# Kernel tuning notes

Hardware: AMD Instinct MI355X
Metric: run time of the kernel (lower is better)

Reference implementation:

```python
import jax, jax.numpy as jnp
import numpy as np

D_MODEL = 1024
NUM_HEADS = 16
HEAD_DIM = D_MODEL // NUM_HEADS


def setup_inputs() -> dict:
    key = jax.random.key(0)
    ks = jax.random.split(key, 10)
    B, SQ, SKV = 4, 2048, 2048
    s = 1.0 / np.sqrt(D_MODEL)
    return {
        "query": jax.random.normal(ks[0], (B, SQ, D_MODEL), jnp.float32),
        "key_value": jax.random.normal(ks[1], (B, SKV, D_MODEL), jnp.float32),
        "Wq": jax.random.normal(ks[2], (D_MODEL, D_MODEL), jnp.float32) * s,
        "bq": jnp.zeros((D_MODEL,), jnp.float32),
        "Wk": jax.random.normal(ks[3], (D_MODEL, D_MODEL), jnp.float32) * s,
        "bk": jnp.zeros((D_MODEL,), jnp.float32),
        "Wv": jax.random.normal(ks[4], (D_MODEL, D_MODEL), jnp.float32) * s,
        "bv": jnp.zeros((D_MODEL,), jnp.float32),
        "Wo": jax.random.normal(ks[5], (D_MODEL, D_MODEL), jnp.float32) * s,
        "bo": jnp.zeros((D_MODEL,), jnp.float32),
    }


def reference(query, key_value, Wq, bq, Wk, bk, Wv, bv, Wo, bo):
    B, SQ, _ = query.shape
    SKV = key_value.shape[1]
    H, Dh = NUM_HEADS, HEAD_DIM
    # projections (torch Linear: x @ W.T + b); split heads -> (B, H, S, Dh)
    Q = (query @ Wq.T + bq).reshape(B, SQ, H, Dh).transpose(0, 2, 1, 3)
    K = (key_value @ Wk.T + bk).reshape(B, SKV, H, Dh).transpose(0, 2, 1, 3)
    V = (key_value @ Wv.T + bv).reshape(B, SKV, H, Dh).transpose(0, 2, 1, 3)
    scale = jnp.asarray(np.sqrt(Dh), query.dtype)
    scores = jnp.einsum("bhqd,bhkd->bhqk", Q, K) / scale
    weights = jax.nn.softmax(scores, axis=-1)  # dropout is identity in eval
    attn = jnp.einsum("bhqk,bhkd->bhqd", weights, V)
    attn = attn.transpose(0, 2, 1, 3).reshape(B, SQ, H * Dh)
    return attn @ Wo.T + bo
```

## Files before the change

kernel.cpp:

```cpp
#include <hip/hip_runtime.h>

#define NH 16
#define DH 64
#define DM 1024
#define SEQ 2048
#define BATCH 4

typedef short s16x8 __attribute__((ext_vector_type(8)));
typedef float f32x4 __attribute__((ext_vector_type(4)));

__device__ __forceinline__ unsigned short f2bf(float f) {
  union { float f; unsigned int u; } v; v.f = f;
  unsigned int u = v.u;
  unsigned int r = (u + 0x7fffu + ((u >> 16) & 1u)) >> 16;
  return (unsigned short)r;
}

__device__ __forceinline__ unsigned int pkbf(float a, float b) {
#if __has_builtin(__builtin_amdgcn_cvt_pk_bf16_f32)
  typedef short v2s __attribute__((ext_vector_type(2)));
  v2s r = __builtin_amdgcn_cvt_pk_bf16_f32(a, b);
  union { v2s v; unsigned int u; } cv; cv.v = r;
  return cv.u;
#else
  return (unsigned int)f2bf(a) | ((unsigned int)f2bf(b) << 16);
#endif
}

__device__ __forceinline__ float fexp2(float x) {
#if __has_builtin(__builtin_amdgcn_exp2f)
  return __builtin_amdgcn_exp2f(x);
#else
  return exp2f(x);
#endif
}

__device__ __forceinline__ void gload_lds16(const void* g, void* l) {
  __builtin_amdgcn_global_load_lds(
      (const __attribute__((address_space(1))) unsigned int*)g,
      (__attribute__((address_space(3))) unsigned int*)l, 16, 0, 0);
}

__global__ void convert_all(const float* __restrict__ q, const float* __restrict__ kv,
                            const float* __restrict__ w0, const float* __restrict__ w1,
                            const float* __restrict__ w2, const float* __restrict__ w3,
                            unsigned short* __restrict__ oq, unsigned short* __restrict__ okv,
                            unsigned short* __restrict__ ow0, unsigned short* __restrict__ ow1,
                            unsigned short* __restrict__ ow2, unsigned short* __restrict__ ow3) {
  const int NQ4 = (BATCH * SEQ * DM) / 4;
  const int NW4 = (DM * DM) / 4;
  const int total = NQ4 * 2 + NW4 * 4;
  for (int i = blockIdx.x * blockDim.x + threadIdx.x; i < total;
       i += gridDim.x * blockDim.x) {
    const float* s; unsigned short* d; int off;
    if (i < NQ4)            { s = q;  d = oq;  off = i; }
    else if (i < 2 * NQ4)   { s = kv; d = okv; off = i - NQ4; }
    else {
      int j = i - 2 * NQ4; int wsel = j / NW4; off = j - wsel * NW4;
      s = (wsel == 0) ? w0 : (wsel == 1) ? w1 : (wsel == 2) ? w2 : w3;
      d = (wsel == 0) ? ow0 : (wsel == 1) ? ow1 : (wsel == 2) ? ow2 : ow3;
    }
    float4 v = *(const float4*)(s + (size_t)off * 4);
    ushort4 o;
    o.x = f2bf(v.x); o.y = f2bf(v.y); o.z = f2bf(v.z); o.w = f2bf(v.w);
    *(ushort4*)(d + (size_t)off * 4) = o;
  }
}

__device__ __forceinline__ void gemm_tile(const unsigned short* __restrict__ X,
                                          const unsigned short* __restrict__ Wt,
                                          unsigned short* As, unsigned short* Bs,
                                          int m0, int n0, f32x4 (*acc)[4]) {
  const int tid = threadIdx.x;
  const int wv_ = tid >> 6, lane = tid & 63;
  const int quad = lane >> 4, c = lane & 15;
  const int wm = (wv_ >> 1) * 64, wn = (wv_ & 1) * 64;
  const int srow = lane >> 3;
  const int scol = ((lane & 7) ^ srow) * 8;

  for (int kt = 0; kt < DM; kt += 64) {
#pragma unroll
    for (int i = 0; i < 4; ++i) {
      int reg = wv_ * 4 + i;
      gload_lds16(X + (size_t)(m0 + reg * 8 + srow) * DM + kt + scol,
                  (void*)(As + reg * 512));
      gload_lds16(Wt + (size_t)(n0 + reg * 8 + srow) * DM + kt + scol,
                  (void*)(Bs + reg * 512));
    }
    __syncthreads();
#pragma unroll
    for (int k2 = 0; k2 < 2; ++k2) {
      s16x8 a[4], b[4];
      int g = k2 * 4 + quad;
#pragma unroll
      for (int t = 0; t < 4; ++t)
        a[t] = *(const s16x8*)(As + (wm + t * 16 + c) * 64 + ((g ^ (c & 7)) * 8));
#pragma unroll
      for (int t = 0; t < 4; ++t)
        b[t] = *(const s16x8*)(Bs + (wn + t * 16 + c) * 64 + ((g ^ (c & 7)) * 8));
#pragma unroll
      for (int tm = 0; tm < 4; ++tm)
#pragma unroll
        for (int tn = 0; tn < 4; ++tn)
          acc[tm][tn] = __builtin_amdgcn_mfma_f32_16x16x32_bf16(
              a[tm], b[tn], acc[tm][tn], 0, 0, 0);
    }
    __syncthreads();
  }
}

__global__ __launch_bounds__(256)
void gemm_qkv(const unsigned short* __restrict__ Xq,
              const unsigned short* __restrict__ Xkv,
              const unsigned short* __restrict__ W0,
              const unsigned short* __restrict__ W1,
              const unsigned short* __restrict__ W2,
              const float* __restrict__ b0, const float* __restrict__ b1,
              const float* __restrict__ b2,
              unsigned short* __restrict__ OQ, unsigned short* __restrict__ OK_,
              unsigned short* __restrict__ OV) {
  __shared__ alignas(16) unsigned short As[128 * 64];
  __shared__ alignas(16) unsigned short Bs[128 * 64];
  const int wg = blockIdx.x;
  const int L = (wg & 7) * 192 + (wg >> 3);
  const int m0 = (L & 63) * 128;
  const int yy = L >> 6;
  const int ysel = yy >> 3;
  const int n0 = (yy & 7) * 128;
  const unsigned short* X = (ysel == 0) ? Xq : Xkv;
  const unsigned short* Wt = (ysel == 0) ? W0 : (ysel == 1) ? W1 : W2;
  const float* bias = (ysel == 0) ? b0 : (ysel == 1) ? b1 : b2;
  unsigned short* Out = (ysel == 0) ? OQ : (ysel == 1) ? OK_ : OV;
  const float scale = (ysel == 0) ? 0.1803368801f : 1.0f;

  f32x4 acc[4][4] = {};
  gemm_tile(X, Wt, As, Bs, m0, n0, acc);

  const int tid = threadIdx.x;
  const int wv_ = tid >> 6, lane = tid & 63;
  const int quad = lane >> 4, c = lane & 15;
  const int wm = (wv_ >> 1) * 64, wn = (wv_ & 1) * 64;
#pragma unroll
  for (int tm = 0; tm < 4; ++tm) {
#pragma unroll
    for (int tn = 0; tn < 4; ++tn) {
      int n = n0 + wn + tn * 16 + c;
      float bv = bias[n];
      int m_base = m0 + wm + tm * 16 + quad * 4;
      if (ysel == 2) {
        int b_ = m_base >> 11, s_ = m_base & 2047, h_ = n >> 6, dh = n & 63;
        size_t idx = (((size_t)(b_ * NH + h_)) * DH + dh) * SEQ + s_;
        ushort4 o4;
        o4.x = f2bf(acc[tm][tn][0] + bv);
        o4.y = f2bf(acc[tm][tn][1] + bv);
        o4.z = f2bf(acc[tm][tn][2] + bv);
        o4.w = f2bf(acc[tm][tn][3] + bv);
        *(ushort4*)(&Out[idx]) = o4;
      } else {
#pragma unroll
        for (int p = 0; p < 4; ++p) {
          int m = m_base + p;
          float val = (acc[tm][tn][p] + bv) * scale;
          int b_ = m >> 11, s_ = m & 2047, h_ = n >> 6, dh = n & 63;
          size_t idx = (((size_t)(b_ * NH + h_)) * SEQ + s_) * DH + dh;
          Out[idx] = f2bf(val);
        }
      }
    }
  }
}

__global__ __launch_bounds__(256)
void gemm_o(const unsigned short* __restrict__ X,
            const unsigned short* __restrict__ Wt,
            const float* __restrict__ bias, float* __restrict__ Out) {
  __shared__ alignas(16) unsigned short As[128 * 64];
  __shared__ alignas(16) unsigned short Bs[128 * 64];
  const int wg = blockIdx.x;
  const int L = (wg & 7) * 64 + (wg >> 3);
  const int m0 = (L & 63) * 128;
  const int n0 = (L >> 6) * 128;
  f32x4 acc[4][4] = {};
  gemm_tile(X, Wt, As, Bs, m0, n0, acc);

  const int tid = threadIdx.x;
  const int wv_ = tid >> 6, lane = tid & 63;
  const int quad = lane >> 4, c = lane & 15;
  const int wm = (wv_ >> 1) * 64, wn = (wv_ & 1) * 64;
#pragma unroll
  for (int tm = 0; tm < 4; ++tm) {
#pragma unroll
    for (int tn = 0; tn < 4; ++tn) {
      int n = n0 + wn + tn * 16 + c;
      float bv = bias[n];
#pragma unroll
      for (int p = 0; p < 4; ++p) {
        int m = m0 + wm + tm * 16 + quad * 4 + p;
        Out[(size_t)m * DM + n] = acc[tm][tn][p] + bv;
      }
    }
  }
}

__global__ __launch_bounds__(512, 2)
void attn_kernel(const unsigned short* __restrict__ Qb,
                 const unsigned short* __restrict__ Kb,
                 const unsigned short* __restrict__ VTb,
                 unsigned short* __restrict__ Ob) {
  __shared__ alignas(16) unsigned short SM[18432];

  const int tid = threadIdx.x, wv_ = tid >> 6, lane = tid & 63;
  const int quad = lane >> 4, c = lane & 15;
  const int wg = blockIdx.x;
  const int bh = (wg & 7) + 8 * ((wg >> 3) >> 2);
  const int qb = (wg >> 3) & 3;
  const unsigned short* Qp = Qb + (size_t)bh * SEQ * DH;
  const unsigned short* Kp = Kb + (size_t)bh * SEQ * DH;
  const unsigned short* Vp = VTb + (size_t)bh * DH * SEQ;
  const int wq0 = qb * 512 + wv_ * 64;

  s16x8 aq[4][2];
#pragma unroll
  for (int t = 0; t < 4; ++t)
#pragma unroll
    for (int k2 = 0; k2 < 2; ++k2)
      aq[t][k2] = *(const s16x8*)(Qp + (size_t)(wq0 + t * 16 + c) * DH +
                                  k2 * 32 + quad * 8);

  f32x4 ot[4][4] = {};
  f32x4 lacc[4] = {};
  s16x8 ones;
  {
    union { s16x8 v; unsigned short u[8]; } o_;
#pragma unroll
    for (int j = 0; j < 8; ++j) o_.u[j] = 0x3F80;
    ones = o_.v;
  }

  const int srow = lane >> 3;
  const int schunk = (lane & 7) ^ srow;

#pragma unroll
  for (int i = 0; i < 2; ++i) {
    int slab = wv_ * 2 + i;
    if (slab < 8) {
      gload_lds16(Kp + (size_t)(slab * 8 + srow) * DH + schunk * 8,
                  (void*)(SM + slab * 512));
    } else {
      int s2 = slab - 8;
      gload_lds16(Vp + (size_t)(s2 * 8 + srow) * SEQ + schunk * 8,
                  (void*)(SM + 8192 + s2 * 512));
    }
  }

  for (int kt = 0; kt < SEQ; kt += 64) {
    const int cur = (kt >> 6) & 1;
    __syncthreads();
    if (kt + 64 < SEQ) {
      const int nxt = cur ^ 1;
#pragma unroll
      for (int i = 0; i < 2; ++i) {
        int slab = wv_ * 2 + i;
        if (slab < 8) {
          gload_lds16(Kp + (size_t)(kt + 64 + slab * 8 + srow) * DH + schunk * 8,
                      (void*)(SM + nxt * 4096 + slab * 512));
        } else {
          int s2 = slab - 8;
          gload_lds16(Vp + (size_t)(s2 * 8 + srow) * SEQ + kt + 64 + schunk * 8,
                      (void*)(SM + 8192 + nxt * 4096 + s2 * 512));
        }
      }
    }
    const unsigned short* K_ = SM + cur * 4096;
    const unsigned short* V_ = SM + 8192 + cur * 4096;

    f32x4 s[4][2][2] = {};
#pragma unroll
    for (int k2 = 0; k2 < 2; ++k2) {
      s16x8 ak[2][2];
#pragma unroll
      for (int jp = 0; jp < 2; ++jp)
#pragma unroll
        for (int h = 0; h < 2; ++h) {
          int r = jp * 32 + ((c >> 2) << 3) + h * 4 + (c & 3);
          int g = k2 * 4 + quad;
          ak[jp][h] = *(const s16x8*)(K_ + r * 64 + ((g ^ (r & 7)) * 8));
        }
#pragma unroll
      for (int t = 0; t < 4; ++t)
#pragma unroll
        for (int jp = 0; jp < 2; ++jp)
#pragma unroll
          for (int h = 0; h < 2; ++h)
            s[t][jp][h] = __builtin_amdgcn_mfma_f32_16x16x32_bf16(
                ak[jp][h], aq[t][k2], s[t][jp][h], 0, 0, 0);
    }

    s16x8 bp[4][2];
#pragma unroll
    for (int t = 0; t < 4; ++t)
#pragma unroll
      for (int jp = 0; jp < 2; ++jp) {
        float e00 = fexp2(s[t][jp][0][0]);
        float e01 = fexp2(s[t][jp][0][1]);
        float e02 = fexp2(s[t][jp][0][2]);
        float e03 = fexp2(s[t][jp][0][3]);
        float e10 = fexp2(s[t][jp][1][0]);
        float e11 = fexp2(s[t][jp][1][1]);
        float e12 = fexp2(s[t][jp][1][2]);
        float e13 = fexp2(s[t][jp][1][3]);
        union { s16x8 v; unsigned int u[4]; } pk;
        pk.u[0] = pkbf(e00, e01);
        pk.u[1] = pkbf(e02, e03);
        pk.u[2] = pkbf(e10, e11);
        pk.u[3] = pkbf(e12, e13);
        bp[t][jp] = pk.v;
        lacc[t] = __builtin_amdgcn_mfma_f32_16x16x32_bf16(
            ones, bp[t][jp], lacc[t], 0, 0, 0);
      }

#pragma unroll
    for (int jp = 0; jp < 2; ++jp)
#pragma unroll
      for (int dt = 0; dt < 4; ++dt) {
        int g = jp * 4 + quad;
        int r = dt * 16 + c;
        s16x8 av = *(const s16x8*)(V_ + r * 64 + ((g ^ (r & 7)) * 8));
#pragma unroll
        for (int t = 0; t < 4; ++t)
          ot[dt][t] = __builtin_amdgcn_mfma_f32_16x16x32_bf16(
              av, bp[t][jp], ot[dt][t], 0, 0, 0);
      }
  }

  __syncthreads();

  const int b_ = bh >> 4, h_ = bh & 15;
  const int ql = lane >> 1, hf = lane & 1;
  unsigned short* Lq = SM + wv_ * (32 * 72);
#pragma unroll
  for (int half = 0; half < 2; ++half) {
    if (half) asm volatile("s_waitcnt lgkmcnt(0)" ::: "memory");
#pragma unroll
    for (int t2 = 0; t2 < 2; ++t2) {
      int t = half * 2 + t2;
      float inv = 1.0f / lacc[t][0];
#pragma unroll
      for (int dt = 0; dt < 4; ++dt) {
        unsigned int w01 = pkbf(ot[dt][t][0] * inv, ot[dt][t][1] * inv);
        unsigned int w23 = pkbf(ot[dt][t][2] * inv, ot[dt][t][3] * inv);
        unsigned short* p = Lq + (t2 * 16 + c) * 72 + dt * 16 + quad * 4;
        *(unsigned int*)(p) = w01;
        *(unsigned int*)(p + 2) = w23;
      }
    }
    const unsigned short* Lr = Lq + ql * 72 + hf * 32;
    unsigned short* Og = Ob + ((size_t)(b_ * SEQ + wq0 + half * 32 + ql)) * DM +
                         h_ * 64 + hf * 32;
#pragma unroll
    for (int j = 0; j < 4; ++j) {
      s16x8 v = *(const s16x8*)(Lr + j * 8);
      *(s16x8*)(Og + j * 8) = v;
    }
  }
}

extern "C" void kernel_launch(void* const* d_in, const int* in_sizes, int n_in,
                              void* d_out, int out_size, void* d_ws, size_t ws_size,
                              hipStream_t stream) {
  const float* q  = (const float*)d_in[0];
  const float* kv = (const float*)d_in[1];
  const float* Wq = (const float*)d_in[2];
  const float* bq = (const float*)d_in[3];
  const float* Wk = (const float*)d_in[4];
  const float* bk = (const float*)d_in[5];
  const float* Wv = (const float*)d_in[6];
  const float* bv = (const float*)d_in[7];
  const float* Wo = (const float*)d_in[8];
  const float* bo = (const float*)d_in[9];

  char* ws = (char*)d_ws;
  const size_t MB = 1024 * 1024;
  unsigned short* q_bf  = (unsigned short*)(ws);
  unsigned short* kv_bf = (unsigned short*)(ws + 16 * MB);
  unsigned short* wq_bf = (unsigned short*)(ws + 32 * MB);
  unsigned short* wk_bf = (unsigned short*)(ws + 34 * MB);
  unsigned short* wv_bf = (unsigned short*)(ws + 36 * MB);
  unsigned short* wo_bf = (unsigned short*)(ws + 38 * MB);
  unsigned short* Qb    = (unsigned short*)(ws + 40 * MB);
  unsigned short* Kb    = (unsigned short*)(ws + 56 * MB);
  unsigned short* VTb   = (unsigned short*)(ws + 72 * MB);
  unsigned short* attn  = (unsigned short*)(ws + 88 * MB);

  convert_all<<<2048, 256, 0, stream>>>(q, kv, Wq, Wk, Wv, Wo,
                                        q_bf, kv_bf, wq_bf, wk_bf, wv_bf, wo_bf);
  gemm_qkv<<<dim3(1536), 256, 0, stream>>>(q_bf, kv_bf, wq_bf, wk_bf, wv_bf,
                                           bq, bk, bv, Qb, Kb, VTb);
  attn_kernel<<<dim3(256), 512, 0, stream>>>(Qb, Kb, VTb, attn);
  gemm_o<<<dim3(512), 256, 0, stream>>>(attn, wo_bf, bo, (float*)d_out);
}
```

Before: 325.7 us.

## Change LDS swizzle for K/V tiles and drop XCD-aware block remapping in GEMMs

Replaces the LDS XOR swizzle for the K and V tiles in attention. The old one XORed the 16-byte chunk index with the row index mod 8; the new one uses a pattern matched to the MFMA read lane mapping (fK, fV) and applies the same pattern on the global-to-LDS store side. The aim is fewer LDS bank conflicts on the fragment reads. Separately, the QKV and output GEMMs go back to a plain 2D grid without the XCD-interleaved block index remap. That may hurt L2 locality across the chiplets.

```diff
diff --git a/kernel.cpp b/kernel.cpp
--- a/kernel.cpp
+++ b/kernel.cpp
@@ -121,12 +121,9 @@
               unsigned short* __restrict__ OV) {
   __shared__ alignas(16) unsigned short As[128 * 64];
   __shared__ alignas(16) unsigned short Bs[128 * 64];
-  const int wg = blockIdx.x;
-  const int L = (wg & 7) * 192 + (wg >> 3);
-  const int m0 = (L & 63) * 128;
-  const int yy = L >> 6;
-  const int ysel = yy >> 3;
-  const int n0 = (yy & 7) * 128;
+  const int m0 = blockIdx.x * 128;
+  const int ysel = blockIdx.y >> 3;
+  const int n0 = (blockIdx.y & 7) * 128;
   const unsigned short* X = (ysel == 0) ? Xq : Xkv;
   const unsigned short* Wt = (ysel == 0) ? W0 : (ysel == 1) ? W1 : W2;
   const float* bias = (ysel == 0) ? b0 : (ysel == 1) ? b1 : b2;
@@ -176,10 +173,8 @@
             const float* __restrict__ bias, float* __restrict__ Out) {
   __shared__ alignas(16) unsigned short As[128 * 64];
   __shared__ alignas(16) unsigned short Bs[128 * 64];
-  const int wg = blockIdx.x;
-  const int L = (wg & 7) * 64 + (wg >> 3);
-  const int m0 = (L & 63) * 128;
-  const int n0 = (L >> 6) * 128;
+  const int m0 = blockIdx.x * 128;
+  const int n0 = blockIdx.y * 128;
   f32x4 acc[4][4] = {};
   gemm_tile(X, Wt, As, Bs, m0, n0, acc);
 
@@ -238,17 +233,22 @@
   }
 
   const int srow = lane >> 3;
-  const int schunk = (lane & 7) ^ srow;
+  const int sbase = (lane & 7) ^ (srow & 3);
+
+  const int fK = (c & 3) | (((c >> 2) & 1) << 2);
+  const int fV = (c & 3) | (((c >> 3) & 1) << 2);
 
 #pragma unroll
   for (int i = 0; i < 2; ++i) {
     int slab = wv_ * 2 + i;
     if (slab < 8) {
-      gload_lds16(Kp + (size_t)(slab * 8 + srow) * DH + schunk * 8,
+      int ch = sbase ^ ((slab & 1) << 2);
+      gload_lds16(Kp + (size_t)(slab * 8 + srow) * DH + ch * 8,
                   (void*)(SM + slab * 512));
     } else {
       int s2 = slab - 8;
-      gload_lds16(Vp + (size_t)(s2 * 8 + srow) * SEQ + schunk * 8,
+      int ch = sbase ^ ((s2 & 1) << 2);
+      gload_lds16(Vp + (size_t)(s2 * 8 + srow) * SEQ + ch * 8,
                   (void*)(SM + 8192 + s2 * 512));
     }
   }
@@ -262,11 +262,13 @@
       for (int i = 0; i < 2; ++i) {
         int slab = wv_ * 2 + i;
         if (slab < 8) {
-          gload_lds16(Kp + (size_t)(kt + 64 + slab * 8 + srow) * DH + schunk * 8,
+          int ch = sbase ^ ((slab & 1) << 2);
+          gload_lds16(Kp + (size_t)(kt + 64 + slab * 8 + srow) * DH + ch * 8,
                       (void*)(SM + nxt * 4096 + slab * 512));
         } else {
           int s2 = slab - 8;
-          gload_lds16(Vp + (size_t)(s2 * 8 + srow) * SEQ + kt + 64 + schunk * 8,
+          int ch = sbase ^ ((s2 & 1) << 2);
+          gload_lds16(Vp + (size_t)(s2 * 8 + srow) * SEQ + kt + 64 + ch * 8,
                       (void*)(SM + 8192 + nxt * 4096 + s2 * 512));
         }
       }
@@ -284,7 +286,7 @@
         for (int h = 0; h < 2; ++h) {
           int r = jp * 32 + ((c >> 2) << 3) + h * 4 + (c & 3);
           int g = k2 * 4 + quad;
-          ak[jp][h] = *(const s16x8*)(K_ + r * 64 + ((g ^ (r & 7)) * 8));
+          ak[jp][h] = *(const s16x8*)(K_ + r * 64 + ((g ^ fK) * 8));
         }
 #pragma unroll
       for (int t = 0; t < 4; ++t)
@@ -325,7 +327,7 @@
       for (int dt = 0; dt < 4; ++dt) {
         int g = jp * 4 + quad;
         int r = dt * 16 + c;
-        s16x8 av = *(const s16x8*)(V_ + r * 64 + ((g ^ (r & 7)) * 8));
+        s16x8 av = *(const s16x8*)(V_ + r * 64 + ((g ^ fV) * 8));
 #pragma unroll
         for (int t = 0; t < 4; ++t)
           ot[dt][t] = __builtin_amdgcn_mfma_f32_16x16x32_bf16(
@@ -394,8 +396,8 @@
 
   convert_all<<<2048, 256, 0, stream>>>(q, kv, Wq, Wk, Wv, Wo,
                                         q_bf, kv_bf, wq_bf, wk_bf, wv_bf, wo_bf);
-  gemm_qkv<<<dim3(1536), 256, 0, stream>>>(q_bf, kv_bf, wq_bf, wk_bf, wv_bf,
-                                           bq, bk, bv, Qb, Kb, VTb);
+  gemm_qkv<<<dim3(64, 24), 256, 0, stream>>>(q_bf, kv_bf, wq_bf, wk_bf, wv_bf,
+                                             bq, bk, bv, Qb, Kb, VTb);
   attn_kernel<<<dim3(256), 512, 0, stream>>>(Qb, Kb, VTb, attn);
-  gemm_o<<<dim3(512), 256, 0, stream>>>(attn, wo_bf, bo, (float*)d_out);
-}
+  gemm_o<<<dim3(64, 8), 256, 0, stream>>>(attn, wo_bf, bo, (float*)d_out);
+}
```

Result: faster. 305.4 us (-6.2%).
